# Kernel tuning notes

Hardware: AMD Instinct MI355X
Metric: run time of the kernel (lower is better)

The kernel has to match this reference:

```python
import jax, jax.numpy as jnp
import numpy as np

B, S, D, H = 2, 2048, 1024, 16
DK = D // H  # 64


def rotate_half(x):
    d = x.shape[-1]
    x1, x2 = x[..., : d // 2], x[..., d // 2 :]
    return jnp.concatenate([-x2, x1], axis=-1)


def apply_rope(q, k):
    # q, k: [B, H, S, DK]
    d_k = q.shape[-1]
    seq_len = q.shape[-2]
    theta = 10000.0 ** (-2.0 / d_k * jnp.arange(d_k // 2, dtype=q.dtype))
    positions = jnp.arange(seq_len, dtype=q.dtype)
    angles = jnp.outer(positions, theta)                    # [S, DK/2]
    cos = jnp.tile(jnp.cos(angles), (1, 2))                 # [S, DK]
    sin = jnp.tile(jnp.sin(angles), (1, 2))
    q = q * cos + rotate_half(q) * sin
    k = k * cos + rotate_half(k) * sin
    return q, k


def setup_inputs() -> dict:
    key = jax.random.key(0)
    ks = jax.random.split(key, 9)
    std = 1.0 / np.sqrt(D)
    x = jax.random.normal(ks[0], (B, S, D), dtype=jnp.float32)
    # mask True = masked (code uses masked_fill(mask, -inf)); causal mask
    mask = jnp.triu(jnp.ones((S, S), dtype=bool), k=1)[None, None, :, :]
    mask = jnp.broadcast_to(mask, (B, 1, S, S))
    Wq = jax.random.uniform(ks[1], (D, D), jnp.float32, -std, std)
    bq = jax.random.uniform(ks[2], (D,), jnp.float32, -std, std)
    Wk = jax.random.uniform(ks[3], (D, D), jnp.float32, -std, std)
    bk = jax.random.uniform(ks[4], (D,), jnp.float32, -std, std)
    Wv = jax.random.uniform(ks[5], (D, D), jnp.float32, -std, std)
    bv = jax.random.uniform(ks[6], (D,), jnp.float32, -std, std)
    Wo = jax.random.uniform(ks[7], (D, D), jnp.float32, -std, std)
    bo = jax.random.uniform(ks[8], (D,), jnp.float32, -std, std)
    return {"x": x, "mask": mask, "Wq": Wq, "bq": bq, "Wk": Wk, "bk": bk,
            "Wv": Wv, "bv": bv, "Wo": Wo, "bo": bo}


def reference(x, mask, Wq, bq, Wk, bk, Wv, bv, Wo, bo):
    b, s, d = x.shape
    # projections -> [B, H, S, DK]
    q = (x @ Wq + bq).reshape(b, s, H, DK).transpose(0, 2, 1, 3)
    k = (x @ Wk + bk).reshape(b, s, H, DK).transpose(0, 2, 1, 3)
    v = (x @ Wv + bv).reshape(b, s, H, DK).transpose(0, 2, 1, 3)
    q, k = apply_rope(q, k)
    scores = jnp.einsum("bhqd,bhkd->bhqk", q, k) / np.sqrt(DK)
    scores = jnp.where(mask, -jnp.inf, scores)
    probs = jax.nn.softmax(scores, axis=-1)
    attn = jnp.einsum("bhqk,bhkd->bhqd", probs, v)
    o = attn.transpose(0, 2, 1, 3).reshape(b, s, H * DK)
    return o @ Wo + bo
```

## Files before the change

### kernel.cpp

```cpp
#include <hip/hip_runtime.h>
#include <hip/hip_bf16.h>
#include <math.h>

typedef __hip_bfloat16 bf16;
typedef __attribute__((ext_vector_type(8))) short short8;
typedef __attribute__((ext_vector_type(4))) short s16x4;
typedef __attribute__((ext_vector_type(4))) float f32x4;

#define B_  2
#define S_  2048
#define D_  1024
#define H_  16
#define DK_ 64

__device__ inline short bfs(float f) { return __builtin_bit_cast(short, __float2bfloat16(f)); }

#define GLL16(gptr, lptr)                                                        \
    __builtin_amdgcn_global_load_lds(                                            \
        (const __attribute__((address_space(1))) void*)(gptr),                   \
        (__attribute__((address_space(3))) void*)(lptr), 16, 0, 0)

#if __has_builtin(__builtin_amdgcn_mfma_f32_16x16x16bf16_1k)
#define MFMA_16x16x16(A, Bv, C) __builtin_amdgcn_mfma_f32_16x16x16bf16_1k(A, Bv, C, 0, 0, 0)
#elif __has_builtin(__builtin_amdgcn_mfma_f32_16x16x16_bf16)
#define MFMA_16x16x16(A, Bv, C) __builtin_amdgcn_mfma_f32_16x16x16_bf16(A, Bv, C, 0, 0, 0)
#else
static __device__ inline f32x4 mfma16_asm(s16x4 a, s16x4 b, f32x4 c) {
    f32x4 d;
    asm volatile("v_mfma_f32_16x16x16_bf16 %0, %1, %2, %3\n\ts_nop 7\n\ts_nop 7"
                 : "=v"(d) : "v"(a), "v"(b), "v"(c));
    return d;
}
#define MFMA_16x16x16(A, Bv, C) mfma16_asm(A, Bv, C)
#endif

__global__ __launch_bounds__(256)
void cvt_x_k(const float* __restrict__ x, bf16* __restrict__ cx)
{
    const size_t g = ((size_t)blockIdx.x * 256 + threadIdx.x) * 4;
    const float4 v = *(const float4*)(x + g);
    s16x4 o = { bfs(v.x), bfs(v.y), bfs(v.z), bfs(v.w) };
    *(s16x4*)(cx + g) = o;
}

__global__ __launch_bounds__(256)
void cvtT_w_k(const float* __restrict__ W0, const float* __restrict__ W1,
              const float* __restrict__ W2, const float* __restrict__ W3,
              bf16* __restrict__ Wt)
{
    __shared__ float Lt[64][65];
    const int z = blockIdx.z;
    const float* W = (z == 0) ? W0 : (z == 1) ? W1 : (z == 2) ? W2 : W3;
    bf16* dst = Wt + (size_t)z * D_ * D_;
    const int k0 = blockIdx.y * 64, n0 = blockIdx.x * 64;
    const int t = threadIdx.x;
    #pragma unroll
    for (int p = 0; p < 4; p++) {
        const int idx = p * 256 + t;
        const int row = idx >> 4, cb = (idx & 15) * 4;
        const float4 v = *(const float4*)(W + (size_t)(k0 + row) * D_ + n0 + cb);
        Lt[cb + 0][row] = v.x; Lt[cb + 1][row] = v.y;
        Lt[cb + 2][row] = v.z; Lt[cb + 3][row] = v.w;
    }
    __syncthreads();
    #pragma unroll
    for (int p = 0; p < 4; p++) {
        const int idx = p * 256 + t;
        const int n = idx >> 4, kb = (idx & 15) * 4;
        s16x4 o = { bfs(Lt[n][kb]), bfs(Lt[n][kb + 1]), bfs(Lt[n][kb + 2]), bfs(Lt[n][kb + 3]) };
        *(s16x4*)(dst + (size_t)(n0 + n) * D_ + k0 + kb) = o;
    }
}

template<int MODE>
__global__ __launch_bounds__(256)
void gemm_k(const bf16* __restrict__ A, const bf16* __restrict__ WtAll,
            const float* __restrict__ b0, const float* __restrict__ b1,
            const float* __restrict__ b2,
            bf16* __restrict__ d0, bf16* __restrict__ d1, bf16* __restrict__ d2,
            float* __restrict__ fout)
{
    constexpr int K = D_;
    const int z = (MODE == 0) ? blockIdx.z : 3;
    const bf16* W = WtAll + (size_t)z * D_ * D_;
    const float* bias = (MODE == 1) ? b0 : ((z == 0) ? b0 : (z == 1) ? b1 : b2);

    __shared__ __align__(16) short As[128 * 32];
    __shared__ __align__(16) short Bs[128 * 32];

    const int m0 = blockIdx.y * 128;
    const int n0 = blockIdx.x * 128;
    const int t = threadIdx.x;
    const int wave = t >> 6, lane = t & 63, quad = lane >> 4, l16 = lane & 15;
    const int wm = (wave >> 1) * 64, wn = (wave & 1) * 64;

    const bf16* gA0 = A + (size_t)(m0 + (t >> 2)) * K + (t & 3) * 8;
    const bf16* gA1 = gA0 + (size_t)64 * K;
    const bf16* gW0 = W + (size_t)(n0 + (t >> 2)) * K + (t & 3) * 8;
    const bf16* gW1 = gW0 + (size_t)64 * K;
    short* lA0 = &As[wave * 512];
    short* lA1 = &As[2048 + wave * 512];
    short* lB0 = &Bs[wave * 512];
    short* lB1 = &Bs[2048 + wave * 512];

    f32x4 acc[4][4] = {};

    for (int k0 = 0; k0 < K; k0 += 32) {
        __syncthreads();
        GLL16(gA0 + k0, lA0);
        GLL16(gA1 + k0, lA1);
        GLL16(gW0 + k0, lB0);
        GLL16(gW1 + k0, lB1);
        __syncthreads();
        short8 af[4], bf[4];
        #pragma unroll
        for (int i = 0; i < 4; i++) af[i] = *(const short8*)&As[(wm + i * 16 + l16) * 32 + quad * 8];
        #pragma unroll
        for (int j = 0; j < 4; j++) bf[j] = *(const short8*)&Bs[(wn + j * 16 + l16) * 32 + quad * 8];
        #pragma unroll
        for (int i = 0; i < 4; i++)
            #pragma unroll
            for (int j = 0; j < 4; j++)
                acc[i][j] = __builtin_amdgcn_mfma_f32_16x16x32_bf16(af[i], bf[j], acc[i][j], 0, 0, 0);
    }

    if (MODE == 1) {
        #pragma unroll
        for (int j = 0; j < 4; j++) {
            const int ncol = n0 + wn + j * 16 + l16;
            const float bb = bias[ncol];
            #pragma unroll
            for (int i = 0; i < 4; i++) {
                const int mbase = m0 + wm + i * 16 + quad * 4;
                #pragma unroll
                for (int r = 0; r < 4; r++)
                    fout[(size_t)(mbase + r) * D_ + ncol] = acc[i][j][r] + bb;
            }
        }
    } else if (z == 2) {
        #pragma unroll
        for (int j = 0; j < 4; j++) {
            const int ncol = n0 + wn + j * 16 + l16;
            const float bb = bias[ncol];
            const int h = ncol >> 6, dk = ncol & 63;
            #pragma unroll
            for (int i = 0; i < 4; i++) {
                const int mbase = m0 + wm + i * 16 + quad * 4;
                #pragma unroll
                for (int r = 0; r < 4; r++) {
                    const int m = mbase + r;
                    const int b = m >> 11, s = m & (S_ - 1);
                    d2[(((size_t)(b * H_ + h)) * DK_ + dk) * S_ + s] = __float2bfloat16(acc[i][j][r] + bb);
                }
            }
        }
    } else {
        bf16* dst = z ? d1 : d0;
        const float sc = z ? 1.0f : 0.125f;
        const int h = (n0 + wn) >> 6;
        #pragma unroll
        for (int j = 0; j < 2; j++) {
            const int dk = j * 16 + l16;
            const float th = exp2f((float)dk * -0.41524101186092029f);
            const float blo = bias[(h << 6) + dk];
            const float bhi = bias[(h << 6) + dk + 32];
            #pragma unroll
            for (int i = 0; i < 4; i++) {
                #pragma unroll
                for (int r = 0; r < 4; r++) {
                    const int m = m0 + wm + i * 16 + quad * 4 + r;
                    const int b = m >> 11, s = m & (S_ - 1);
                    float sn, cs;
                    sincosf((float)s * th, &sn, &cs);
                    const float v1 = acc[i][j][r] + blo;
                    const float v2 = acc[i][j + 2][r] + bhi;
                    bf16* p = dst + (((size_t)(b * H_ + h)) * S_ + s) * DK_;
                    p[dk]      = __float2bfloat16((v1 * cs - v2 * sn) * sc);
                    p[dk + 32] = __float2bfloat16((v2 * cs + v1 * sn) * sc);
                }
            }
        }
    }
}

__global__ __launch_bounds__(256)
void attn_k(const bf16* __restrict__ q_ws, const bf16* __restrict__ k_ws,
            const bf16* __restrict__ vt_ws, bf16* __restrict__ attn_ws)
{
    __shared__ __align__(16) short Ks[64 * 72];
    __shared__ __align__(16) short Vts[64 * 72];

    const int bh = blockIdx.y;
    const int t = threadIdx.x;
    const int wave = t >> 6, lane = t & 63, quad = lane >> 4, l16 = lane & 15;
    const bf16* Kb = k_ws + (size_t)bh * S_ * DK_;
    const bf16* Vb = vt_ws + (size_t)bh * DK_ * S_;
    const int b = bh >> 4, h = bh & 15;

    for (int pass = 0; pass < 2; pass++) {
        const int qt = pass ? (31 - (int)blockIdx.x) : (int)blockIdx.x;
        const int q0 = qt * 64;

        const bf16* Qb = q_ws + ((size_t)bh * S_ + q0 + wave * 16) * DK_;
        const short8 qf0 = *(const short8*)(Qb + (size_t)l16 * DK_ + quad * 8);
        const short8 qf1 = *(const short8*)(Qb + (size_t)l16 * DK_ + 32 + quad * 8);

        float l_acc = 0.0f;
        f32x4 ot[4] = {};

        for (int kt = 0; kt <= qt; kt++) {
            __syncthreads();
            #pragma unroll
            for (int p = 0; p < 2; p++) {
                const int idx = p * 256 + t;
                const int row = idx >> 3, cb = (idx & 7) * 8;
                *(float4*)&Ks[row * 72 + cb]  = *(const float4*)(Kb + (size_t)(kt * 64 + row) * DK_ + cb);
                *(float4*)&Vts[row * 72 + cb] = *(const float4*)(Vb + (size_t)row * S_ + kt * 64 + cb);
            }
            __syncthreads();

            const bool diag = (kt == qt);
            const int kkmax = diag ? wave : 3;
            for (int kk = 0; kk <= kkmax; kk++) {
                const short8 kf0 = *(const short8*)&Ks[(kk * 16 + l16) * 72 + quad * 8];
                const short8 kf1 = *(const short8*)&Ks[(kk * 16 + l16) * 72 + 32 + quad * 8];
                f32x4 st = {};
                st = __builtin_amdgcn_mfma_f32_16x16x32_bf16(kf0, qf0, st, 0, 0, 0);
                st = __builtin_amdgcn_mfma_f32_16x16x32_bf16(kf1, qf1, st, 0, 0, 0);

                s16x4 pt;
                float psum = 0.0f;
                #pragma unroll
                for (int r = 0; r < 4; r++) {
                    const bool masked = diag && (kk == wave) && (quad * 4 + r > l16);
                    const float p = masked ? 0.0f : __expf(st[r] - 8.0f);
                    psum += p;
                    pt[r] = bfs(p);
                }
                l_acc += psum;

                #pragma unroll
                for (int dt = 0; dt < 4; dt++) {
                    const s16x4 vf = *(const s16x4*)&Vts[(dt * 16 + l16) * 72 + kk * 16 + quad * 4];
                    ot[dt] = MFMA_16x16x16(vf, pt, ot[dt]);
                }
            }
        }

        l_acc += __shfl_xor(l_acc, 16, 64);
        l_acc += __shfl_xor(l_acc, 32, 64);
        const float inv = 1.0f / l_acc;
        const int srow = q0 + wave * 16 + l16;
        bf16* orow = attn_ws + ((size_t)(b * S_ + srow)) * D_ + h * 64;
        #pragma unroll
        for (int dt = 0; dt < 4; dt++) {
            s16x4 o4 = { bfs(ot[dt][0] * inv), bfs(ot[dt][1] * inv),
                         bfs(ot[dt][2] * inv), bfs(ot[dt][3] * inv) };
            *(s16x4*)(orow + dt * 16 + quad * 4) = o4;
        }
    }
}

extern "C" void kernel_launch(void* const* d_in, const int* in_sizes, int n_in,
                              void* d_out, int out_size, void* d_ws, size_t ws_size,
                              hipStream_t stream)
{
    (void)out_size; (void)ws_size;
    const float* x = nullptr;
    const float* W[4] = {nullptr, nullptr, nullptr, nullptr};
    const float* bias[4] = {nullptr, nullptr, nullptr, nullptr};
    int wi = 0, bi = 0;
    for (int i = 0; i < n_in; i++) {
        const int sz = in_sizes[i];
        if (sz == B_ * S_ * D_ && x == nullptr) x = (const float*)d_in[i];
        else if (sz == D_ * D_ && wi < 4) W[wi++] = (const float*)d_in[i];
        else if (sz == D_ && bi < 4) bias[bi++] = (const float*)d_in[i];
    }

    bf16* ws = (bf16*)d_ws;
    const size_t SEG = (size_t)B_ * S_ * D_;
    bf16* canonX  = ws;
    bf16* Wt      = ws + SEG;
    bf16* k_ws    = ws + 2 * SEG;
    bf16* vt_ws   = ws + 3 * SEG;
    bf16* attn_ws = canonX;
    bf16* q_ws    = (bf16*)d_out;

    cvt_x_k<<<(B_ * S_ * D_) / 4 / 256, 256, 0, stream>>>(x, canonX);

    cvtT_w_k<<<dim3(16, 16, 4), 256, 0, stream>>>(W[0], W[1], W[2], W[3], Wt);

    gemm_k<0><<<dim3(D_ / 128, (B_ * S_) / 128, 3), 256, 0, stream>>>(
        canonX, Wt, bias[0], bias[1], bias[2], q_ws, k_ws, vt_ws, nullptr);

    attn_k<<<dim3(16, B_ * H_), 256, 0, stream>>>(q_ws, k_ws, vt_ws, attn_ws);

    gemm_k<1><<<dim3(D_ / 128, (B_ * S_) / 128, 1), 256, 0, stream>>>(
        attn_ws, Wt, bias[3], nullptr, nullptr, nullptr, nullptr, nullptr,
        (float*)d_out);
}
```

Before: 250.2 us.

## Share K/V tile loads across paired query tiles and fuse prep kernels

The attention kernel now processes the paired query tiles (qt and 31-qt) together in a single K/V loop. Each loaded K/V tile therefore serves both query tiles, which roughly halves the K/V global loads and barrier rounds for the shorter tile. The input and weight conversion kernels merge into one launch, and the block-to-(bh, pair) mapping is reordered. The softmax switches to exp2f by folding log2(e) into the Q scale, at the cost of higher register pressure from holding two sets of accumulators.

```diff
diff --git a/kernel.cpp b/kernel.cpp
--- a/kernel.cpp
+++ b/kernel.cpp
@@ -12,6 +12,9 @@
 #define D_  1024
 #define H_  16
 #define DK_ 64
+
+#define QSCALE 0.18033688011112043f
+#define EXPOFF 11.541560327111707f
 
 __device__ inline short bfs(float f) { return __builtin_bit_cast(short, __float2bfloat16(f)); }
 
@@ -35,25 +38,28 @@
 #endif
 
 __global__ __launch_bounds__(256)
-void cvt_x_k(const float* __restrict__ x, bf16* __restrict__ cx)
-{
-    const size_t g = ((size_t)blockIdx.x * 256 + threadIdx.x) * 4;
-    const float4 v = *(const float4*)(x + g);
-    s16x4 o = { bfs(v.x), bfs(v.y), bfs(v.z), bfs(v.w) };
-    *(s16x4*)(cx + g) = o;
-}
-
-__global__ __launch_bounds__(256)
-void cvtT_w_k(const float* __restrict__ W0, const float* __restrict__ W1,
-              const float* __restrict__ W2, const float* __restrict__ W3,
-              bf16* __restrict__ Wt)
-{
+void prep_k(const float* __restrict__ x,
+            const float* __restrict__ W0, const float* __restrict__ W1,
+            const float* __restrict__ W2, const float* __restrict__ W3,
+            bf16* __restrict__ cx, bf16* __restrict__ Wt)
+{
+    const int z = blockIdx.z;
+    const int t = threadIdx.x;
+    if (z == 4) {
+        const int bid = blockIdx.y * 16 + blockIdx.x;
+        #pragma unroll
+        for (int i = 0; i < 16; i++) {
+            const size_t g = ((size_t)bid * 256 + t) * 4 + (size_t)i * 262144;
+            const float4 v = *(const float4*)(x + g);
+            s16x4 o = { bfs(v.x), bfs(v.y), bfs(v.z), bfs(v.w) };
+            *(s16x4*)(cx + g) = o;
+        }
+        return;
+    }
     __shared__ float Lt[64][65];
-    const int z = blockIdx.z;
     const float* W = (z == 0) ? W0 : (z == 1) ? W1 : (z == 2) ? W2 : W3;
     bf16* dst = Wt + (size_t)z * D_ * D_;
     const int k0 = blockIdx.y * 64, n0 = blockIdx.x * 64;
-    const int t = threadIdx.x;
     #pragma unroll
     for (int p = 0; p < 4; p++) {
         const int idx = p * 256 + t;
@@ -156,7 +162,7 @@
         }
     } else {
         bf16* dst = z ? d1 : d0;
-        const float sc = z ? 1.0f : 0.125f;
+        const float sc = z ? 1.0f : QSCALE;
         const int h = (n0 + wn) >> 6;
         #pragma unroll
         for (int j = 0; j < 2; j++) {
@@ -183,6 +189,39 @@
     }
 }
 
+__device__ __forceinline__
+void attn_tile(const short* __restrict__ Ks, const short* __restrict__ Vts,
+               const short8 qf0, const short8 qf1,
+               f32x4* ot, float& l_acc,
+               const bool diag, const int wave, const int quad, const int l16)
+{
+    const int kkmax = diag ? wave : 3;
+    for (int kk = 0; kk <= kkmax; kk++) {
+        const short8 kf0 = *(const short8*)&Ks[(kk * 16 + l16) * 72 + quad * 8];
+        const short8 kf1 = *(const short8*)&Ks[(kk * 16 + l16) * 72 + 32 + quad * 8];
+        f32x4 st = {};
+        st = __builtin_amdgcn_mfma_f32_16x16x32_bf16(kf0, qf0, st, 0, 0, 0);
+        st = __builtin_amdgcn_mfma_f32_16x16x32_bf16(kf1, qf1, st, 0, 0, 0);
+
+        s16x4 pt;
+        float psum = 0.0f;
+        #pragma unroll
+        for (int r = 0; r < 4; r++) {
+            const bool masked = diag && (kk == wave) && (quad * 4 + r > l16);
+            const float p = masked ? 0.0f : exp2f(st[r] - EXPOFF);
+            psum += p;
+            pt[r] = bfs(p);
+        }
+        l_acc += psum;
+
+        #pragma unroll
+        for (int dt = 0; dt < 4; dt++) {
+            const s16x4 vf = *(const s16x4*)&Vts[(dt * 16 + l16) * 72 + kk * 16 + quad * 4];
+            ot[dt] = MFMA_16x16x16(vf, pt, ot[dt]);
+        }
+    }
+}
+
 __global__ __launch_bounds__(256)
 void attn_k(const bf16* __restrict__ q_ws, const bf16* __restrict__ k_ws,
             const bf16* __restrict__ vt_ws, bf16* __restrict__ attn_ws)
@@ -190,63 +229,47 @@
     __shared__ __align__(16) short Ks[64 * 72];
     __shared__ __align__(16) short Vts[64 * 72];
 
-    const int bh = blockIdx.y;
+    const int linear = (int)blockIdx.y * 16 + (int)blockIdx.x;
+    const int bh = linear & 31;
+    const int pr = linear >> 5;
+    const int qtA = pr, qtB = 31 - pr;
     const int t = threadIdx.x;
-    const int wave = t >> 6, lane = t & 63, quad = lane >> 4, l16 = lane & 15;
+    const int wave = t >> 6, quad = (t & 63) >> 4, l16 = t & 15;
     const bf16* Kb = k_ws + (size_t)bh * S_ * DK_;
     const bf16* Vb = vt_ws + (size_t)bh * DK_ * S_;
     const int b = bh >> 4, h = bh & 15;
 
-    for (int pass = 0; pass < 2; pass++) {
-        const int qt = pass ? (31 - (int)blockIdx.x) : (int)blockIdx.x;
-        const int q0 = qt * 64;
-
-        const bf16* Qb = q_ws + ((size_t)bh * S_ + q0 + wave * 16) * DK_;
-        const short8 qf0 = *(const short8*)(Qb + (size_t)l16 * DK_ + quad * 8);
-        const short8 qf1 = *(const short8*)(Qb + (size_t)l16 * DK_ + 32 + quad * 8);
-
-        float l_acc = 0.0f;
-        f32x4 ot[4] = {};
-
-        for (int kt = 0; kt <= qt; kt++) {
-            __syncthreads();
-            #pragma unroll
-            for (int p = 0; p < 2; p++) {
-                const int idx = p * 256 + t;
-                const int row = idx >> 3, cb = (idx & 7) * 8;
-                *(float4*)&Ks[row * 72 + cb]  = *(const float4*)(Kb + (size_t)(kt * 64 + row) * DK_ + cb);
-                *(float4*)&Vts[row * 72 + cb] = *(const float4*)(Vb + (size_t)row * S_ + kt * 64 + cb);
-            }
-            __syncthreads();
-
-            const bool diag = (kt == qt);
-            const int kkmax = diag ? wave : 3;
-            for (int kk = 0; kk <= kkmax; kk++) {
-                const short8 kf0 = *(const short8*)&Ks[(kk * 16 + l16) * 72 + quad * 8];
-                const short8 kf1 = *(const short8*)&Ks[(kk * 16 + l16) * 72 + 32 + quad * 8];
-                f32x4 st = {};
-                st = __builtin_amdgcn_mfma_f32_16x16x32_bf16(kf0, qf0, st, 0, 0, 0);
-                st = __builtin_amdgcn_mfma_f32_16x16x32_bf16(kf1, qf1, st, 0, 0, 0);
-
-                s16x4 pt;
-                float psum = 0.0f;
-                #pragma unroll
-                for (int r = 0; r < 4; r++) {
-                    const bool masked = diag && (kk == wave) && (quad * 4 + r > l16);
-                    const float p = masked ? 0.0f : __expf(st[r] - 8.0f);
-                    psum += p;
-                    pt[r] = bfs(p);
-                }
-                l_acc += psum;
-
-                #pragma unroll
-                for (int dt = 0; dt < 4; dt++) {
-                    const s16x4 vf = *(const s16x4*)&Vts[(dt * 16 + l16) * 72 + kk * 16 + quad * 4];
-                    ot[dt] = MFMA_16x16x16(vf, pt, ot[dt]);
-                }
-            }
-        }
-
+    const bf16* QbA = q_ws + ((size_t)bh * S_ + qtA * 64 + wave * 16) * DK_;
+    const bf16* QbB = q_ws + ((size_t)bh * S_ + qtB * 64 + wave * 16) * DK_;
+    const short8 qfA0 = *(const short8*)(QbA + (size_t)l16 * DK_ + quad * 8);
+    const short8 qfA1 = *(const short8*)(QbA + (size_t)l16 * DK_ + 32 + quad * 8);
+    const short8 qfB0 = *(const short8*)(QbB + (size_t)l16 * DK_ + quad * 8);
+    const short8 qfB1 = *(const short8*)(QbB + (size_t)l16 * DK_ + 32 + quad * 8);
+
+    float lA = 0.0f, lB = 0.0f;
+    f32x4 otA[4] = {}, otB[4] = {};
+
+    for (int kt = 0; kt <= qtB; kt++) {
+        __syncthreads();
+        #pragma unroll
+        for (int p = 0; p < 2; p++) {
+            const int idx = p * 256 + t;
+            const int row = idx >> 3, cb = (idx & 7) * 8;
+            *(float4*)&Ks[row * 72 + cb]  = *(const float4*)(Kb + (size_t)(kt * 64 + row) * DK_ + cb);
+            *(float4*)&Vts[row * 72 + cb] = *(const float4*)(Vb + (size_t)row * S_ + kt * 64 + cb);
+        }
+        __syncthreads();
+
+        if (kt <= qtA)
+            attn_tile(Ks, Vts, qfA0, qfA1, otA, lA, kt == qtA, wave, quad, l16);
+        attn_tile(Ks, Vts, qfB0, qfB1, otB, lB, kt == qtB, wave, quad, l16);
+    }
+
+    #pragma unroll
+    for (int which = 0; which < 2; which++) {
+        float l_acc = which ? lB : lA;
+        f32x4* ot = which ? otB : otA;
+        const int q0 = (which ? qtB : qtA) * 64;
         l_acc += __shfl_xor(l_acc, 16, 64);
         l_acc += __shfl_xor(l_acc, 32, 64);
         const float inv = 1.0f / l_acc;
@@ -286,9 +309,7 @@
     bf16* attn_ws = canonX;
     bf16* q_ws    = (bf16*)d_out;
 
-    cvt_x_k<<<(B_ * S_ * D_) / 4 / 256, 256, 0, stream>>>(x, canonX);
-
-    cvtT_w_k<<<dim3(16, 16, 4), 256, 0, stream>>>(W[0], W[1], W[2], W[3], Wt);
+    prep_k<<<dim3(16, 16, 5), 256, 0, stream>>>(x, W[0], W[1], W[2], W[3], canonX, Wt);
 
     gemm_k<0><<<dim3(D_ / 128, (B_ * S_) / 128, 3), 256, 0, stream>>>(
         canonX, Wt, bias[0], bias[1], bias[2], q_ws, k_ws, vt_ws, nullptr);
```

New measurement: 240.4 us. 1.04x faster.
